# Optimization experiments

Hardware: AMD Instinct MI355X
Metric: run time of the kernel (lower is better)

## Reference

```python
import jax, jax.numpy as jnp
import numpy as np

B, D, N, PT_DEPTH = 1024, 1024, 128, 28
TOPK_FRAC = 0.25
NOISE_EPS = 0.01

def setup_inputs() -> dict:
    key = jax.random.key(0)
    ks = jax.random.split(key, 10)
    s = 0.02
    return {
        "prompt_embeddings": jax.random.normal(ks[0], (PT_DEPTH, N, D), jnp.float32) * s,
        "w1": jax.random.normal(ks[1], (D, 1), jnp.float32) * s,      # Linear(1, D) weight [out,in]
        "b1": jnp.zeros((D,), jnp.float32),
        "w2": jax.random.normal(ks[2], (D, D), jnp.float32) * s,      # Linear(D, D)
        "b2": jnp.zeros((D,), jnp.float32),
        "gate_w": jax.random.normal(ks[3], (N, D + 1), jnp.float32) * s,  # Linear(D+1, N)
        "gate_b": jnp.zeros((N,), jnp.float32),
        "w_noise": jax.random.normal(ks[4], (D, N), jnp.float32) * s,
        "noise": jax.random.normal(ks[5], (B, N), jnp.float32),
        "timestep": jax.random.randint(ks[6], (B,), 0, PT_DEPTH, jnp.int64),
    }

def reference(prompt_embeddings, w1, b1, w2, b2, gate_w, gate_b, w_noise, noise, timestep):
    step = timestep[0]  # scalar index, like timestep[0].item()
    t = timestep.astype(jnp.float32)[:, None]                    # [B, 1]
    # timestep embedder: Linear -> SiLU -> Linear
    t_embed = jax.nn.silu(t @ w1.T + b1) @ w2.T + b2             # [B, D]
    prompts = prompt_embeddings[step]                            # [N, D]
    # noisy top-k gating
    depth_col = jnp.full((t_embed.shape[0], 1), 0.0, jnp.float32) + step.astype(jnp.float32)
    gate_in = jnp.concatenate([t_embed, depth_col], axis=-1)     # [B, D+1]
    clean_logits = gate_in @ gate_w.T + gate_b                   # [B, N]
    noise_std = jax.nn.softplus(t_embed @ w_noise) + NOISE_EPS   # [B, N]
    noisy_logits = clean_logits + noise * noise_std
    k = min(int(TOPK_FRAC * N) + 1, N)                           # 33 (static)
    top_logits, top_idx = jax.lax.top_k(noisy_logits, k)
    top_k_gates = jax.nn.softmax(top_logits[:, : k - 1], axis=-1)  # [B, k-1]
    rows = jnp.arange(noisy_logits.shape[0])[:, None]
    gates = jnp.zeros_like(noisy_logits).at[rows, top_idx[:, : k - 1]].set(top_k_gates)  # [B, N]
    out = prompts[None, :, :] * gates[:, :, None]                # [B, N, D]
    return out, t_embed
```

## Files before the change

### kernel.cpp

```cpp
#include <hip/hip_runtime.h>
#include <math.h>

#define B_ 1024
#define D_ 1024
#define N_ 128
#define PT_ 28
#define KSEL 32
#define NOISE_EPS_ 0.01f

__global__ __launch_bounds__(256) void embed_kernel(
    const float* __restrict__ w1, const float* __restrict__ b1,
    const float* __restrict__ w2, const float* __restrict__ b2,
    float* __restrict__ ue)
{
    __shared__ float h[D_];
    const int s = blockIdx.x;
    const int tid = threadIdx.x;
    const float sf = (float)s;
    for (int d = tid; d < D_; d += 256) {
        float x = sf * w1[d] + b1[d];
        h[d] = x / (1.0f + expf(-x));
    }
    __syncthreads();
    const int i = blockIdx.y * 256 + tid;
    const float4* row = (const float4*)(w2 + (size_t)i * D_);
    float acc = 0.0f;
    for (int d = 0; d < D_ / 4; ++d) {
        float4 u = row[d];
        const int d4 = d * 4;
        acc += h[d4 + 0] * u.x + h[d4 + 1] * u.y + h[d4 + 2] * u.z + h[d4 + 3] * u.w;
    }
    ue[(size_t)s * D_ + i] = acc + b2[i];
}

__global__ __launch_bounds__(256) void gate_precompute_kernel(
    const float* __restrict__ gate_w, const float* __restrict__ gate_b,
    const float* __restrict__ w_noise, const int* __restrict__ timestep,
    const float* __restrict__ ue, float* __restrict__ uclean, float* __restrict__ unstd)
{
    __shared__ float te[D_];
    __shared__ float pc[2][N_];
    __shared__ float pn[2][N_];
    const int s = blockIdx.x;
    const int tid = threadIdx.x;
    for (int d = tid; d < D_; d += 256) te[d] = ue[(size_t)s * D_ + d];
    __syncthreads();
    const int n = tid & (N_ - 1);
    const int half = tid >> 7;
    const int d0 = half * (D_ / 2);
    const float* grow = gate_w + (size_t)n * (D_ + 1) + d0;
    float cl = 0.0f, nz = 0.0f;
    for (int d = 0; d < D_ / 2; ++d) {
        float tv = te[d0 + d];
        cl += tv * grow[d];
        nz += tv * w_noise[(size_t)(d0 + d) * N_ + n];
    }
    pc[half][n] = cl; pn[half][n] = nz;
    __syncthreads();
    if (tid < N_) {
        const int step = timestep[0];
        float cl2 = pc[0][tid] + pc[1][tid]
                  + (float)step * gate_w[(size_t)tid * (D_ + 1) + D_]
                  + gate_b[tid];
        uclean[s * N_ + tid] = cl2;
        float nz2 = pn[0][tid] + pn[1][tid];
        float sp = (nz2 > 20.0f) ? nz2 : log1pf(expf(nz2));
        unstd[s * N_ + tid] = sp + NOISE_EPS_;
    }
}

__global__ __launch_bounds__(256) void out_kernel(
    const float* __restrict__ pe,
    const float* __restrict__ noise,
    const int* __restrict__ timestep,
    const float* __restrict__ ue, const float* __restrict__ uclean,
    const float* __restrict__ unstd,
    float* __restrict__ out0, float* __restrict__ out1)
{
    __shared__ float noisy[N_];
    __shared__ float gates[N_];
    __shared__ float inv_sum;
    const int b = blockIdx.x;
    const int tid = threadIdx.x;
    const int tb = timestep[b];
    const int step = timestep[0];

    const float* uer = ue + (size_t)tb * D_;
    for (int i = tid; i < D_; i += 256)
        out1[(size_t)b * D_ + i] = uer[i];

    if (tid < N_) {
        noisy[tid] = uclean[tb * N_ + tid]
                   + noise[(size_t)b * N_ + tid] * unstd[tb * N_ + tid];
    }
    __syncthreads();
    if (tid < N_) {
        const float v = noisy[tid];
        int rank = 0; float mx = -INFINITY;
        for (int m = 0; m < N_; ++m) {
            float u = noisy[m];
            mx = fmaxf(mx, u);
            rank += ((u > v) || (u == v && m < tid)) ? 1 : 0;
        }
        gates[tid] = (rank < KSEL) ? expf(v - mx) : 0.0f;
    }
    __syncthreads();
    if (tid == 0) {
        float s = 0.0f;
        for (int m = 0; m < N_; ++m) s += gates[m];
        inv_sum = 1.0f / s;
    }
    __syncthreads();
    if (tid < N_) gates[tid] *= inv_sum;
    __syncthreads();

    const float4* __restrict__ psrc = (const float4*)(pe + (size_t)step * N_ * D_);
    float4* __restrict__ pdst = (float4*)(out0 + (size_t)b * N_ * D_);
    const int NV = N_ * D_ / 4;
    for (int idx = tid; idx < NV; idx += 256) {
        const int n = idx >> 8;
        const float g = gates[n];
        float4 o;
        if (g != 0.0f) {
            float4 u = psrc[idx];
            o.x = u.x * g; o.y = u.y * g; o.z = u.z * g; o.w = u.w * g;
        } else {
            o.x = 0.0f; o.y = 0.0f; o.z = 0.0f; o.w = 0.0f;
        }
        pdst[idx] = o;
    }
}

extern "C" void kernel_launch(void* const* d_in, const int* in_sizes, int n_in,
                              void* d_out, int out_size, void* d_ws, size_t ws_size,
                              hipStream_t stream) {
    (void)in_sizes; (void)n_in; (void)out_size; (void)ws_size;
    const float* pe      = (const float*)d_in[0];
    const float* w1      = (const float*)d_in[1];
    const float* b1      = (const float*)d_in[2];
    const float* w2      = (const float*)d_in[3];
    const float* b2      = (const float*)d_in[4];
    const float* gate_w  = (const float*)d_in[5];
    const float* gate_b  = (const float*)d_in[6];
    const float* w_noise = (const float*)d_in[7];
    const float* noise   = (const float*)d_in[8];
    const int*   ts      = (const int*)d_in[9];

    float* ws     = (float*)d_ws;
    float* ue     = ws;
    float* uclean = ue + PT_ * D_;
    float* unstd  = uclean + PT_ * N_;

    float* out0 = (float*)d_out;
    float* out1 = out0 + (size_t)B_ * N_ * D_;

    hipLaunchKernelGGL(embed_kernel, dim3(PT_, 4), dim3(256), 0, stream,
                       w1, b1, w2, b2, ue);
    hipLaunchKernelGGL(gate_precompute_kernel, dim3(PT_), dim3(256), 0, stream,
                       gate_w, gate_b, w_noise, ts, ue, uclean, unstd);
    hipLaunchKernelGGL(out_kernel, dim3(B_), dim3(256), 0, stream,
                       pe, noise, ts, ue, uclean, unstd, out0, out1);
}
```

Before: 623.4 us.

## Coalesce GEMV reads with wave reductions and use nontemporal output stores

```diff
diff --git a/kernel.cpp b/kernel.cpp
--- a/kernel.cpp
+++ b/kernel.cpp
@@ -8,12 +8,14 @@
 #define KSEL 32
 #define NOISE_EPS_ 0.01f
 
+typedef float fx4 __attribute__((ext_vector_type(4)));
+
 __global__ __launch_bounds__(256) void embed_kernel(
     const float* __restrict__ w1, const float* __restrict__ b1,
     const float* __restrict__ w2, const float* __restrict__ b2,
     float* __restrict__ ue)
 {
-    __shared__ float h[D_];
+    __shared__ __align__(16) float h[D_];
     const int s = blockIdx.x;
     const int tid = threadIdx.x;
     const float sf = (float)s;
@@ -22,15 +24,23 @@
         h[d] = x / (1.0f + expf(-x));
     }
     __syncthreads();
-    const int i = blockIdx.y * 256 + tid;
-    const float4* row = (const float4*)(w2 + (size_t)i * D_);
-    float acc = 0.0f;
-    for (int d = 0; d < D_ / 4; ++d) {
-        float4 u = row[d];
-        const int d4 = d * 4;
-        acc += h[d4 + 0] * u.x + h[d4 + 1] * u.y + h[d4 + 2] * u.z + h[d4 + 3] * u.w;
+    const int wave = tid >> 6;
+    const int lane = tid & 63;
+    const fx4* __restrict__ h4 = (const fx4*)h;
+    for (int j = 0; j < 32; ++j) {
+        const int i = blockIdx.y * 128 + wave * 32 + j;
+        const fx4* __restrict__ row = (const fx4*)(w2 + (size_t)i * D_);
+        float acc = 0.0f;
+        #pragma unroll
+        for (int k = 0; k < 4; ++k) {
+            fx4 u  = row[k * 64 + lane];
+            fx4 hv = h4 [k * 64 + lane];
+            acc += u.x * hv.x + u.y * hv.y + u.z * hv.z + u.w * hv.w;
+        }
+        #pragma unroll
+        for (int off = 32; off; off >>= 1) acc += __shfl_down(acc, off, 64);
+        if (lane == 0) ue[(size_t)s * D_ + i] = acc + b2[i];
     }
-    ue[(size_t)s * D_ + i] = acc + b2[i];
 }
 
 __global__ __launch_bounds__(256) void gate_precompute_kernel(
@@ -38,32 +48,45 @@
     const float* __restrict__ w_noise, const int* __restrict__ timestep,
     const float* __restrict__ ue, float* __restrict__ uclean, float* __restrict__ unstd)
 {
-    __shared__ float te[D_];
-    __shared__ float pc[2][N_];
-    __shared__ float pn[2][N_];
+    __shared__ __align__(16) float te[D_];
+    __shared__ float pcl[N_];
+    __shared__ float pnz[2][N_];
     const int s = blockIdx.x;
     const int tid = threadIdx.x;
     for (int d = tid; d < D_; d += 256) te[d] = ue[(size_t)s * D_ + d];
     __syncthreads();
-    const int n = tid & (N_ - 1);
-    const int half = tid >> 7;
-    const int d0 = half * (D_ / 2);
-    const float* grow = gate_w + (size_t)n * (D_ + 1) + d0;
-    float cl = 0.0f, nz = 0.0f;
-    for (int d = 0; d < D_ / 2; ++d) {
-        float tv = te[d0 + d];
-        cl += tv * grow[d];
-        nz += tv * w_noise[(size_t)(d0 + d) * N_ + n];
+    const int wave = tid >> 6;
+    const int lane = tid & 63;
+
+    for (int j = 0; j < 32; ++j) {
+        const int n = wave * 32 + j;
+        const float* __restrict__ grow = gate_w + (size_t)n * (D_ + 1);
+        float acc = 0.0f;
+        #pragma unroll
+        for (int k = 0; k < 16; ++k)
+            acc += grow[k * 64 + lane] * te[k * 64 + lane];
+        #pragma unroll
+        for (int off = 32; off; off >>= 1) acc += __shfl_down(acc, off, 64);
+        if (lane == 0) pcl[n] = acc;
     }
-    pc[half][n] = cl; pn[half][n] = nz;
+
+    {
+        const int n = (wave & 1) * 64 + lane;
+        const int dbase = (wave >> 1) * 512;
+        float acc = 0.0f;
+        for (int d = 0; d < 512; ++d)
+            acc += te[dbase + d] * w_noise[(size_t)(dbase + d) * N_ + n];
+        pnz[wave >> 1][n] = acc;
+    }
     __syncthreads();
+
     if (tid < N_) {
         const int step = timestep[0];
-        float cl2 = pc[0][tid] + pc[1][tid]
+        float cl2 = pcl[tid]
                   + (float)step * gate_w[(size_t)tid * (D_ + 1) + D_]
                   + gate_b[tid];
         uclean[s * N_ + tid] = cl2;
-        float nz2 = pn[0][tid] + pn[1][tid];
+        float nz2 = pnz[0][tid] + pnz[1][tid];
         float sp = (nz2 > 20.0f) ? nz2 : log1pf(expf(nz2));
         unstd[s * N_ + tid] = sp + NOISE_EPS_;
     }
@@ -85,15 +108,19 @@
     const int tb = timestep[b];
     const int step = timestep[0];
 
-    const float* uer = ue + (size_t)tb * D_;
-    for (int i = tid; i < D_; i += 256)
-        out1[(size_t)b * D_ + i] = uer[i];
-
     if (tid < N_) {
         noisy[tid] = uclean[tb * N_ + tid]
                    + noise[(size_t)b * N_ + tid] * unstd[tb * N_ + tid];
     }
+
+    {
+        const fx4* __restrict__ uer = (const fx4*)(ue + (size_t)tb * D_);
+        fx4* __restrict__ o1 = (fx4*)(out1 + (size_t)b * D_);
+        for (int i = tid; i < D_ / 4; i += 256)
+            __builtin_nontemporal_store(uer[i], o1 + i);
+    }
     __syncthreads();
+
     if (tid < N_) {
         const float v = noisy[tid];
         int rank = 0; float mx = -INFINITY;
@@ -105,29 +132,29 @@
         gates[tid] = (rank < KSEL) ? expf(v - mx) : 0.0f;
     }
     __syncthreads();
-    if (tid == 0) {
-        float s = 0.0f;
-        for (int m = 0; m < N_; ++m) s += gates[m];
-        inv_sum = 1.0f / s;
+    if (tid < 64) {
+        float s2 = gates[tid] + gates[tid + 64];
+        #pragma unroll
+        for (int off = 32; off; off >>= 1) s2 += __shfl_down(s2, off, 64);
+        if (tid == 0) inv_sum = 1.0f / s2;
     }
     __syncthreads();
     if (tid < N_) gates[tid] *= inv_sum;
     __syncthreads();
 
-    const float4* __restrict__ psrc = (const float4*)(pe + (size_t)step * N_ * D_);
-    float4* __restrict__ pdst = (float4*)(out0 + (size_t)b * N_ * D_);
-    const int NV = N_ * D_ / 4;
-    for (int idx = tid; idx < NV; idx += 256) {
-        const int n = idx >> 8;
-        const float g = gates[n];
-        float4 o;
+    const fx4* __restrict__ psrc = (const fx4*)(pe + (size_t)step * N_ * D_);
+    fx4* __restrict__ pdst = (fx4*)(out0 + (size_t)b * N_ * D_);
+    for (int it = 0; it < N_; ++it) {
+        const float g = gates[it];
+        const int idx = it * 256 + tid;
+        fx4 o;
         if (g != 0.0f) {
-            float4 u = psrc[idx];
-            o.x = u.x * g; o.y = u.y * g; o.z = u.z * g; o.w = u.w * g;
+            fx4 u = psrc[idx];
+            o = u * g;
         } else {
-            o.x = 0.0f; o.y = 0.0f; o.z = 0.0f; o.w = 0.0f;
+            o = (fx4)0.0f;
         }
-        pdst[idx] = o;
+        __builtin_nontemporal_store(o, pdst + idx);
     }
 }
 
@@ -154,7 +181,7 @@
     float* out0 = (float*)d_out;
     float* out1 = out0 + (size_t)B_ * N_ * D_;
 
-    hipLaunchKernelGGL(embed_kernel, dim3(PT_, 4), dim3(256), 0, stream,
+    hipLaunchKernelGGL(embed_kernel, dim3(PT_, 8), dim3(256), 0, stream,
                        w1, b1, w2, b2, ue);
     hipLaunchKernelGGL(gate_precompute_kernel, dim3(PT_), dim3(256), 0, stream,
                        gate_w, gate_b, w_noise, ts, ue, uclean, unstd);
```

Result: no change. 628.9 us (+0.9%).
